# Performance work log

Hardware: AMD Instinct MI355X
Metric: run time of the kernel (lower is better)

The kernel has to match this reference:

```python
import jax, jax.numpy as jnp
import numpy as np

H_DIM = 768
N_HEADS = 12
SEQ = 4096
MLP_RATIO = 4
EPS = 1e-5


def layernorm(x, g, b):
    mu = jnp.mean(x, axis=-1, keepdims=True)
    var = jnp.var(x, axis=-1, keepdims=True)
    return (x - mu) * jax.lax.rsqrt(var + EPS) * g + b


def setup_inputs() -> dict:
    key = jax.random.key(0)
    ks = jax.random.split(key, 16)
    C, F = H_DIM, MLP_RATIO * H_DIM
    s = 1.0 / np.sqrt(C)
    inp = {
        "x": jax.random.normal(ks[0], (1, SEQ, C), dtype=jnp.float32),
        "Wq": jax.random.normal(ks[1], (C, C), dtype=jnp.float32) * s,
        "bq": jnp.zeros((C,), jnp.float32),
        "Wk": jax.random.normal(ks[2], (C, C), dtype=jnp.float32) * s,
        "bk": jnp.zeros((C,), jnp.float32),
        "Wv": jax.random.normal(ks[3], (C, C), dtype=jnp.float32) * s,
        "bv": jnp.zeros((C,), jnp.float32),
        "Wo": jax.random.normal(ks[4], (C, C), dtype=jnp.float32) * s,
        "bo": jnp.zeros((C,), jnp.float32),
        "ln1_g": jnp.ones((C,), jnp.float32),
        "ln1_b": jnp.zeros((C,), jnp.float32),
        "W1": jax.random.normal(ks[5], (C, F), dtype=jnp.float32) * s,
        "b1": jnp.zeros((F,), jnp.float32),
        "W2": jax.random.normal(ks[6], (F, C), dtype=jnp.float32) * (1.0 / np.sqrt(F)),
        "b2": jnp.zeros((C,), jnp.float32),
        "ln2_g": jnp.ones((C,), jnp.float32),
        "ln2_b": jnp.zeros((C,), jnp.float32),
    }
    return inp


def reference(x, Wq, bq, Wk, bk, Wv, bv, Wo, bo, ln1_g, ln1_b, W1, b1, W2, b2, ln2_g, ln2_b):
    B, T, C = x.shape
    N, D = N_HEADS, C // N_HEADS

    # --- masked self-attention (naive, materializes T x T scores) ---
    q = (x @ Wq + bq).reshape(B, T, N, D).transpose(0, 2, 1, 3)  # [B,N,T,D]
    k = (x @ Wk + bk).reshape(B, T, N, D).transpose(0, 2, 1, 3)
    v = (x @ Wv + bv).reshape(B, T, N, D).transpose(0, 2, 1, 3)

    logits = jnp.einsum("bntd,bnsd->bnts", q, k) / jnp.sqrt(jnp.float32(D))
    causal = jnp.tril(jnp.ones((T, T), dtype=bool))  # True where allowed
    logits = jnp.where(causal, logits, -jnp.inf)
    attn = jax.nn.softmax(logits, axis=-1)
    out = jnp.einsum("bnts,bnsd->bntd", attn, v)
    out = out.transpose(0, 2, 1, 3).reshape(B, T, C)
    attn_out = out @ Wo + bo

    # --- post-norm residual + MLP ---
    h = layernorm(x + attn_out, ln1_g, ln1_b)
    mlp = jax.nn.gelu(h @ W1 + b1, approximate=False) @ W2 + b2
    y = layernorm(h + mlp, ln2_g, ln2_b)
    return y
```

## Files before the change

### kernel.cpp

```cpp
#include <hip/hip_runtime.h>
#include <hip/hip_bf16.h>
#include <math.h>

#define T_SEQ 4096
#define C_DIM 768
#define N_HEADS 12
#define D_HEAD 64
#define F_DIM 3072
#define EPS 1e-5f
#define QSCALE 0.18033688011112042f

typedef __attribute__((ext_vector_type(8))) short short8;
typedef __attribute__((ext_vector_type(4))) float f32x4;

__device__ __forceinline__ void gload_lds16(const void* g, void* lds) {
    __builtin_amdgcn_global_load_lds(
        (const __attribute__((address_space(1))) unsigned int*)g,
        (__attribute__((address_space(3))) unsigned int*)lds, 16, 0, 0);
}

__launch_bounds__(256)
__global__ void transpose_w4(const float* __restrict__ Wq, const float* __restrict__ Wk,
                             const float* __restrict__ Wv, const float* __restrict__ Wo,
                             __hip_bfloat16* __restrict__ Wqkv_t,
                             __hip_bfloat16* __restrict__ Wo_t) {
    __shared__ float tile[64][65];
    const int z = blockIdx.z;
    const float* W = (z == 0) ? Wq : (z == 1) ? Wk : (z == 2) ? Wv : Wo;
    __hip_bfloat16* Wt = (z < 3) ? (Wqkv_t + (size_t)z * C_DIM * C_DIM) : Wo_t;
    const int k0 = blockIdx.x * 64;
    const int n0 = blockIdx.y * 64;
    const int tid = threadIdx.x;
    const int c = tid & 63;
    const int r0 = (tid >> 6) * 16;
    #pragma unroll
    for (int i = 0; i < 16; ++i)
        tile[r0 + i][c] = W[(size_t)(k0 + r0 + i) * C_DIM + n0 + c];
    __syncthreads();
    #pragma unroll
    for (int i = 0; i < 16; ++i)
        Wt[(size_t)(n0 + r0 + i) * C_DIM + k0 + c] = __float2bfloat16(tile[c][r0 + i]);
}

__launch_bounds__(256)
__global__ void transpose_w(const float* __restrict__ W, __hip_bfloat16* __restrict__ Wt,
                            int K, int N) {
    __shared__ float tile[64][65];
    const int k0 = blockIdx.x * 64;
    const int n0 = blockIdx.y * 64;
    const int tid = threadIdx.x;
    const int c = tid & 63;
    const int r0 = (tid >> 6) * 16;
    #pragma unroll
    for (int i = 0; i < 16; ++i)
        tile[r0 + i][c] = W[(size_t)(k0 + r0 + i) * N + n0 + c];
    __syncthreads();
    #pragma unroll
    for (int i = 0; i < 16; ++i)
        Wt[(size_t)(n0 + r0 + i) * K + k0 + c] = __float2bfloat16(tile[c][r0 + i]);
}

__launch_bounds__(256)
__global__ void transpose_v(const __hip_bfloat16* __restrict__ V,
                            __hip_bfloat16* __restrict__ Vt) {
    __shared__ __hip_bfloat16 tile[64][65];
    const int t0 = blockIdx.x * 64;
    const int c0 = blockIdx.y * 64;
    const int tid = threadIdx.x;
    const int c = tid & 63;
    const int r0 = (tid >> 6) * 16;
    #pragma unroll
    for (int i = 0; i < 16; ++i)
        tile[r0 + i][c] = V[(size_t)(t0 + r0 + i) * C_DIM + c0 + c];
    __syncthreads();
    #pragma unroll
    for (int i = 0; i < 16; ++i)
        Vt[(size_t)(c0 + r0 + i) * T_SEQ + t0 + c] = tile[c][r0 + i];
}

__launch_bounds__(256)
__global__ void concat_bias(const float* __restrict__ bq, const float* __restrict__ bk,
                            const float* __restrict__ bv, float* __restrict__ o) {
    const int i = blockIdx.x * 256 + threadIdx.x;
    if (i < C_DIM) {
        o[i] = bq[i];
        o[C_DIM + i] = bk[i];
        o[2 * C_DIM + i] = bv[i];
    }
}

__launch_bounds__(256)
__global__ void f32_to_bf16_vec(const float* __restrict__ in, __hip_bfloat16* __restrict__ out,
                                int n4) {
    const int i = blockIdx.x * 256 + threadIdx.x;
    if (i < n4) {
        const float4 v = *reinterpret_cast<const float4*>(&in[(size_t)i * 4]);
        ushort4 u;
        u.x = __bfloat16_as_ushort(__float2bfloat16(v.x));
        u.y = __bfloat16_as_ushort(__float2bfloat16(v.y));
        u.z = __bfloat16_as_ushort(__float2bfloat16(v.z));
        u.w = __bfloat16_as_ushort(__float2bfloat16(v.w));
        *reinterpret_cast<ushort4*>(&out[(size_t)i * 4]) = u;
    }
}

#define GBK 64

template<int MODE, int TM, int TN>
__launch_bounds__(256)
__global__ void gemm_mfma(const __hip_bfloat16* __restrict__ A,
                          const __hip_bfloat16* __restrict__ Bt,
                          const float* __restrict__ bias,
                          float* __restrict__ outf,
                          __hip_bfloat16* __restrict__ outq,
                          __hip_bfloat16* __restrict__ outk,
                          __hip_bfloat16* __restrict__ outv,
                          int M, int N, int K) {
    constexpr int WM = TM / 2, WN = TN / 2;
    constexpr int FM = WM / 16, FN = WN / 16;
    constexpr int AISS = TM / 32, BISS = TN / 32;

    __shared__ __hip_bfloat16 As[TM][GBK];
    __shared__ __hip_bfloat16 Bs[TN][GBK];

    const int tid = threadIdx.x;
    const int l   = tid & 63;
    const int w   = tid >> 6;
    const int lr  = l & 15;
    const int lg  = l >> 4;
    const int wr  = w >> 1;
    const int wc  = w & 1;
    const int bm  = blockIdx.y * TM;
    const int bn  = blockIdx.x * TN;

    const int srow  = l >> 3;
    const int skoff = (l & 7) * 8;

    f32x4 acc[FM][FN];
    #pragma unroll
    for (int m = 0; m < FM; ++m)
        #pragma unroll
        for (int n = 0; n < FN; ++n)
            acc[m][n] = {0.f, 0.f, 0.f, 0.f};

    for (int k0 = 0; k0 < K; k0 += GBK) {
        if (k0) __syncthreads();
        #pragma unroll
        for (int i = 0; i < AISS; ++i) {
            const int rb = (w * AISS + i) * 8;
            gload_lds16(&A[(size_t)(bm + rb + srow) * K + k0 + skoff], &As[rb][0]);
        }
        #pragma unroll
        for (int i = 0; i < BISS; ++i) {
            const int rb = (w * BISS + i) * 8;
            gload_lds16(&Bt[(size_t)(bn + rb + srow) * K + k0 + skoff], &Bs[rb][0]);
        }
        __syncthreads();

        #pragma unroll
        for (int kk = 0; kk < 2; ++kk) {
            short8 af[FM], bf[FN];
            #pragma unroll
            for (int m = 0; m < FM; ++m)
                af[m] = *reinterpret_cast<const short8*>(
                    &As[wr * WM + m * 16 + lr][kk * 32 + lg * 8]);
            #pragma unroll
            for (int n = 0; n < FN; ++n)
                bf[n] = *reinterpret_cast<const short8*>(
                    &Bs[wc * WN + n * 16 + lr][kk * 32 + lg * 8]);
            #pragma unroll
            for (int m = 0; m < FM; ++m)
                #pragma unroll
                for (int n = 0; n < FN; ++n)
                    acc[m][n] = __builtin_amdgcn_mfma_f32_16x16x32_bf16(af[m], bf[n], acc[m][n], 0, 0, 0);
        }
    }

    #pragma unroll
    for (int m = 0; m < FM; ++m) {
        #pragma unroll
        for (int rr = 0; rr < 4; ++rr) {
            const int row = bm + wr * WM + m * 16 + lg * 4 + rr;
            #pragma unroll
            for (int n = 0; n < FN; ++n) {
                const int col = bn + wc * WN + n * 16 + lr;
                float v = acc[m][n][rr] + bias[col];
                if constexpr (MODE == 0) {
                    outf[(size_t)row * N + col] = v;
                } else if constexpr (MODE == 1) {
                    v = 0.5f * v * (1.0f + erff(v * 0.70710678118654752f));
                    outq[(size_t)row * N + col] = __float2bfloat16(v);
                } else {
                    if (col < C_DIM)
                        outq[(size_t)row * C_DIM + col] = __float2bfloat16(v * QSCALE);
                    else if (col < 2 * C_DIM)
                        outk[(size_t)row * C_DIM + (col - C_DIM)] = __float2bfloat16(v);
                    else
                        outv[(size_t)row * C_DIM + (col - 2 * C_DIM)] = __float2bfloat16(v);
                }
            }
        }
    }
}

#define QBLK 64
#define KVB 128

__launch_bounds__(256)
__global__ void attn_mfma(const __hip_bfloat16* __restrict__ q,
                          const __hip_bfloat16* __restrict__ k,
                          const __hip_bfloat16* __restrict__ vt,
                          __hip_bfloat16* __restrict__ o) {
    __shared__ __hip_bfloat16 Ks[2][KVB][64];
    __shared__ __hip_bfloat16 Vts[2][D_HEAD][KVB];
    __shared__ __hip_bfloat16 Ps[4][16][KVB];

    const int tid  = threadIdx.x;
    const int wid  = tid >> 6;
    const int lane = tid & 63;
    const int lr   = lane & 15;
    const int lg   = lane >> 4;

    const int h  = blockIdx.x;
    const int q0 = T_SEQ - QBLK - blockIdx.y * QBLK;
    const int qw = q0 + wid * 16;

    const int ksrc = 8 * ((lane & 7) ^ (lane >> 3));
    const int kr   = lane >> 3;
    const int vr   = lane >> 4;
    const int vs   = lane & 15;

    short8 aq[2];
    #pragma unroll
    for (int kk = 0; kk < 2; ++kk)
        aq[kk] = *reinterpret_cast<const short8*>(
            &q[(size_t)(qw + lr) * C_DIM + h * D_HEAD + kk * 32 + lg * 8]);

    f32x4 o_acc[4];
    #pragma unroll
    for (int dc = 0; dc < 4; ++dc) o_acc[dc] = {0.f, 0.f, 0.f, 0.f};
    float m_run[4], l_part[4];
    #pragma unroll
    for (int r = 0; r < 4; ++r) { m_run[r] = -1e30f; l_part[r] = 0.f; }

    auto stage = [&](int buf, int s0) {
        #pragma unroll
        for (int i = 0; i < 4; ++i) {
            const int rb = wid * 32 + i * 8;
            gload_lds16(&k[(size_t)(s0 + rb + kr) * C_DIM + h * D_HEAD + ksrc],
                        &Ks[buf][rb][0]);
        }
        #pragma unroll
        for (int i = 0; i < 4; ++i) {
            const int vb = wid * 16 + i * 4;
            const int vsrc = 8 * (vs ^ (i * 4 + vr));
            gload_lds16(&vt[(size_t)(h * D_HEAD + vb + vr) * T_SEQ + s0 + vsrc],
                        &Vts[buf][vb][0]);
        }
    };

    const int n_tiles = (q0 + QBLK + KVB - 1) / KVB;

    stage(0, 0);
    __syncthreads();

    for (int t = 0; t < n_tiles; ++t) {
        const int cur = t & 1;
        if (t + 1 < n_tiles) stage(cur ^ 1, (t + 1) * KVB);

        f32x4 s_acc[8];
        __builtin_amdgcn_s_setprio(1);
        #pragma unroll
        for (int c = 0; c < 8; ++c) {
            s_acc[c] = {0.f, 0.f, 0.f, 0.f};
            #pragma unroll
            for (int kk = 0; kk < 2; ++kk) {
                const short8 bk8 = *reinterpret_cast<const short8*>(
                    &Ks[cur][c * 16 + lr][8 * ((4 * kk + lg) ^ (lr & 7))]);
                s_acc[c] = __builtin_amdgcn_mfma_f32_16x16x32_bf16(aq[kk], bk8, s_acc[c], 0, 0, 0);
            }
        }
        __builtin_amdgcn_s_setprio(0);

        if (t == n_tiles - 1) {
            const int s0 = t * KVB;
            #pragma unroll
            for (int c = 0; c < 8; ++c)
                #pragma unroll
                for (int r = 0; r < 4; ++r) {
                    const int sg = s0 + c * 16 + lr;
                    const int qg = qw + lg * 4 + r;
                    if (sg > qg) s_acc[c][r] = -1e30f;
                }
        }

        float pm[4];
        #pragma unroll
        for (int r = 0; r < 4; ++r) {
            const float m0 = fmaxf(fmaxf(s_acc[0][r], s_acc[1][r]),
                                   fmaxf(s_acc[2][r], s_acc[3][r]));
            const float m1 = fmaxf(fmaxf(s_acc[4][r], s_acc[5][r]),
                                   fmaxf(s_acc[6][r], s_acc[7][r]));
            pm[r] = fmaxf(m0, m1);
        }
        const float need = fmaxf(fmaxf(pm[0] - m_run[0], pm[1] - m_run[1]),
                                 fmaxf(pm[2] - m_run[2], pm[3] - m_run[3]));
        if (!__all(need <= 8.0f)) {
            #pragma unroll
            for (int r = 0; r < 4; ++r) {
                float nm = pm[r];
                #pragma unroll
                for (int off = 1; off < 16; off <<= 1)
                    nm = fmaxf(nm, __shfl_xor(nm, off));
                nm = fmaxf(nm, m_run[r]);
                const float corr = __builtin_amdgcn_exp2f(m_run[r] - nm);
                m_run[r] = nm;
                l_part[r] *= corr;
                #pragma unroll
                for (int dc = 0; dc < 4; ++dc) o_acc[dc][r] *= corr;
            }
        }
        #pragma unroll
        for (int r = 0; r < 4; ++r) {
            const int qrow = lg * 4 + r;
            float ls = 0.f;
            #pragma unroll
            for (int c = 0; c < 8; ++c) {
                const float pv = __builtin_amdgcn_exp2f(s_acc[c][r] - m_run[r]);
                ls += pv;
                const int slot = (2 * c + (lr >> 3)) ^ qrow;
                Ps[wid][qrow][slot * 8 + (lr & 7)] = __float2bfloat16(pv);
            }
            l_part[r] += ls;
        }

        short8 ap[4];
        #pragma unroll
        for (int kk = 0; kk < 4; ++kk)
            ap[kk] = *reinterpret_cast<const short8*>(
                &Ps[wid][lr][8 * ((4 * kk + lg) ^ lr)]);
        __builtin_amdgcn_s_setprio(1);
        #pragma unroll
        for (int dc = 0; dc < 4; ++dc)
            #pragma unroll
            for (int kk = 0; kk < 4; ++kk) {
                const short8 bv8 = *reinterpret_cast<const short8*>(
                    &Vts[cur][dc * 16 + lr][8 * ((4 * kk + lg) ^ lr)]);
                o_acc[dc] = __builtin_amdgcn_mfma_f32_16x16x32_bf16(ap[kk], bv8, o_acc[dc], 0, 0, 0);
            }
        __builtin_amdgcn_s_setprio(0);

        __syncthreads();
    }

    #pragma unroll
    for (int r = 0; r < 4; ++r) {
        #pragma unroll
        for (int off = 1; off < 16; off <<= 1)
            l_part[r] += __shfl_xor(l_part[r], off);
    }

    #pragma unroll
    for (int dc = 0; dc < 4; ++dc)
        #pragma unroll
        for (int r = 0; r < 4; ++r)
            o[(size_t)(qw + lg * 4 + r) * C_DIM + h * D_HEAD + dc * 16 + lr] =
                __float2bfloat16(o_acc[dc][r] / l_part[r]);
}

template<bool WB16>
__launch_bounds__(256)
__global__ void add_ln(const float* __restrict__ a, const float* __restrict__ b,
                       const float* __restrict__ g, const float* __restrict__ beta,
                       float* __restrict__ outf, __hip_bfloat16* __restrict__ outb) {
    const int row = blockIdx.x;
    const int tid = threadIdx.x;
    const size_t rb = (size_t)row * C_DIM;

    float x[3];
    #pragma unroll
    for (int i = 0; i < 3; ++i) {
        const int c = tid + 256 * i;
        x[i] = a[rb + c] + b[rb + c];
    }

    float s = x[0] + x[1] + x[2];
    float s2 = x[0] * x[0] + x[1] * x[1] + x[2] * x[2];

    #pragma unroll
    for (int off = 32; off; off >>= 1) {
        s  += __shfl_xor(s, off);
        s2 += __shfl_xor(s2, off);
    }

    __shared__ float red[10];
    const int wave = tid >> 6;
    const int lane = tid & 63;
    if (lane == 0) { red[wave] = s; red[4 + wave] = s2; }
    __syncthreads();
    if (tid == 0) {
        const float ts  = red[0] + red[1] + red[2] + red[3];
        const float ts2 = red[4] + red[5] + red[6] + red[7];
        const float mu = ts * (1.0f / C_DIM);
        const float var = ts2 * (1.0f / C_DIM) - mu * mu;
        red[8] = mu;
        red[9] = rsqrtf(var + EPS);
    }
    __syncthreads();
    const float mu = red[8];
    const float rstd = red[9];

    #pragma unroll
    for (int i = 0; i < 3; ++i) {
        const int c = tid + 256 * i;
        const float v = (x[i] - mu) * rstd * g[c] + beta[c];
        outf[rb + c] = v;
        if constexpr (WB16) outb[rb + c] = __float2bfloat16(v);
    }
}

extern "C" void kernel_launch(void* const* d_in, const int* in_sizes, int n_in,
                              void* d_out, int out_size, void* d_ws, size_t ws_size,
                              hipStream_t stream) {
    const float* x     = (const float*)d_in[0];
    const float* Wq    = (const float*)d_in[1];
    const float* bq    = (const float*)d_in[2];
    const float* Wk    = (const float*)d_in[3];
    const float* bk    = (const float*)d_in[4];
    const float* Wv    = (const float*)d_in[5];
    const float* bv    = (const float*)d_in[6];
    const float* Wo    = (const float*)d_in[7];
    const float* bo    = (const float*)d_in[8];
    const float* ln1_g = (const float*)d_in[9];
    const float* ln1_b = (const float*)d_in[10];
    const float* W1    = (const float*)d_in[11];
    const float* b1    = (const float*)d_in[12];
    const float* W2    = (const float*)d_in[13];
    const float* b2    = (const float*)d_in[14];
    const float* ln2_g = (const float*)d_in[15];
    const float* ln2_b = (const float*)d_in[16];

    float* out = (float*)d_out;

    char* wsb = (char*)d_ws;
    const size_t TCb16 = (size_t)T_SEQ * C_DIM * 2;
    __hip_bfloat16* xb  = (__hip_bfloat16*)(wsb);
    __hip_bfloat16* qb  = (__hip_bfloat16*)(wsb + TCb16);
    __hip_bfloat16* kb  = (__hip_bfloat16*)(wsb + 2 * TCb16);
    __hip_bfloat16* vtb = (__hip_bfloat16*)(wsb + 3 * TCb16);
    __hip_bfloat16* mid = (__hip_bfloat16*)(wsb);
    float* proj = (float*)(wsb + 4 * TCb16);
    __hip_bfloat16* vb = (__hip_bfloat16*)proj;
    float* mlpo = proj;
    __hip_bfloat16* obuf = (__hip_bfloat16*)(wsb + 4 * TCb16 + 12582912);
    __hip_bfloat16* hb   = obuf;
    float* hbuf = (float*)(wsb + 4 * TCb16 + 12582912 + TCb16);
    char* we = wsb + 4 * TCb16 + 12582912 + TCb16 + 12582912;
    __hip_bfloat16* Wqkv_t = (__hip_bfloat16*)(we);
    __hip_bfloat16* Wo_t   = (__hip_bfloat16*)(we + 3538944);
    __hip_bfloat16* W1_t   = (__hip_bfloat16*)(we + 3538944 + 1179648);
    __hip_bfloat16* W2_t   = (__hip_bfloat16*)(we + 3538944 + 1179648 + 4718592);
    float* bqkv            = (float*)(we + 3538944 + 1179648 + 2 * 4718592);

    const dim3 blk256(256);

    transpose_w4<<<dim3(12, 12, 4), blk256, 0, stream>>>(Wq, Wk, Wv, Wo, Wqkv_t, Wo_t);
    transpose_w<<<dim3(12, 48), blk256, 0, stream>>>(W1, W1_t, C_DIM, F_DIM);
    transpose_w<<<dim3(48, 12), blk256, 0, stream>>>(W2, W2_t, F_DIM, C_DIM);
    concat_bias<<<dim3(3), blk256, 0, stream>>>(bq, bk, bv, bqkv);
    f32_to_bf16_vec<<<dim3(3072), blk256, 0, stream>>>(x, xb, T_SEQ * C_DIM / 4);

    gemm_mfma<2, 128, 128><<<dim3(3 * C_DIM / 128, T_SEQ / 128), blk256, 0, stream>>>(
        xb, Wqkv_t, bqkv, nullptr, qb, kb, vb, T_SEQ, 3 * C_DIM, C_DIM);

    transpose_v<<<dim3(T_SEQ / 64, C_DIM / 64), blk256, 0, stream>>>(vb, vtb);

    attn_mfma<<<dim3(N_HEADS, T_SEQ / QBLK), blk256, 0, stream>>>(qb, kb, vtb, obuf);

    gemm_mfma<0, 64, 64><<<dim3(C_DIM / 64, T_SEQ / 64), blk256, 0, stream>>>(
        obuf, Wo_t, bo, proj, nullptr, nullptr, nullptr, T_SEQ, C_DIM, C_DIM);

    add_ln<true><<<dim3(T_SEQ), blk256, 0, stream>>>(x, proj, ln1_g, ln1_b, hbuf, hb);

    gemm_mfma<1, 128, 128><<<dim3(F_DIM / 128, T_SEQ / 128), blk256, 0, stream>>>(
        hb, W1_t, b1, nullptr, mid, nullptr, nullptr, T_SEQ, F_DIM, C_DIM);

    gemm_mfma<0, 64, 64><<<dim3(C_DIM / 64, T_SEQ / 64), blk256, 0, stream>>>(
        mid, W2_t, b2, mlpo, nullptr, nullptr, nullptr, T_SEQ, C_DIM, F_DIM);

    add_ln<false><<<dim3(T_SEQ), blk256, 0, stream>>>(hbuf, mlpo, ln2_g, ln2_b, out, nullptr);
}
```

Measured before the change: 336.3 us.

## Fuse prep kernels, add split-K to output GEMMs, and XCD-swizzle block order

The weight transposes, x conversion and bias concat are merged into one prep_all launch, which removes several small launches. The Wo and W2 GEMMs (N=768) now use split-K=2 with two fp32 partial buffers that add_ln sums, which doubles the block count. The QKV and W1 GEMMs remap block IDs across 8 chunks, which looks aimed at MI355X's XCD round-robin dispatch so that blocks sharing A/B tiles run on the same L2. The cost is extra fp32 partial-buffer traffic and a larger workspace.

```diff
diff --git a/kernel.cpp b/kernel.cpp
--- a/kernel.cpp
+++ b/kernel.cpp
@@ -20,44 +20,58 @@
 }
 
 __launch_bounds__(256)
-__global__ void transpose_w4(const float* __restrict__ Wq, const float* __restrict__ Wk,
-                             const float* __restrict__ Wv, const float* __restrict__ Wo,
-                             __hip_bfloat16* __restrict__ Wqkv_t,
-                             __hip_bfloat16* __restrict__ Wo_t) {
-    __shared__ float tile[64][65];
-    const int z = blockIdx.z;
-    const float* W = (z == 0) ? Wq : (z == 1) ? Wk : (z == 2) ? Wv : Wo;
-    __hip_bfloat16* Wt = (z < 3) ? (Wqkv_t + (size_t)z * C_DIM * C_DIM) : Wo_t;
-    const int k0 = blockIdx.x * 64;
-    const int n0 = blockIdx.y * 64;
+__global__ void prep_all(const float* __restrict__ Wq, const float* __restrict__ Wk,
+                         const float* __restrict__ Wv, const float* __restrict__ Wo,
+                         const float* __restrict__ W1, const float* __restrict__ W2,
+                         const float* __restrict__ x,
+                         const float* __restrict__ bq, const float* __restrict__ bk,
+                         const float* __restrict__ bv,
+                         __hip_bfloat16* __restrict__ Wqkv_t, __hip_bfloat16* __restrict__ Wo_t,
+                         __hip_bfloat16* __restrict__ W1_t, __hip_bfloat16* __restrict__ W2_t,
+                         __hip_bfloat16* __restrict__ xb, float* __restrict__ bqkv) {
+    const int b = blockIdx.x;
     const int tid = threadIdx.x;
-    const int c = tid & 63;
-    const int r0 = (tid >> 6) * 16;
-    #pragma unroll
-    for (int i = 0; i < 16; ++i)
-        tile[r0 + i][c] = W[(size_t)(k0 + r0 + i) * C_DIM + n0 + c];
-    __syncthreads();
-    #pragma unroll
-    for (int i = 0; i < 16; ++i)
-        Wt[(size_t)(n0 + r0 + i) * C_DIM + k0 + c] = __float2bfloat16(tile[c][r0 + i]);
-}
-
-__launch_bounds__(256)
-__global__ void transpose_w(const float* __restrict__ W, __hip_bfloat16* __restrict__ Wt,
-                            int K, int N) {
-    __shared__ float tile[64][65];
-    const int k0 = blockIdx.x * 64;
-    const int n0 = blockIdx.y * 64;
-    const int tid = threadIdx.x;
-    const int c = tid & 63;
-    const int r0 = (tid >> 6) * 16;
-    #pragma unroll
-    for (int i = 0; i < 16; ++i)
-        tile[r0 + i][c] = W[(size_t)(k0 + r0 + i) * N + n0 + c];
-    __syncthreads();
-    #pragma unroll
-    for (int i = 0; i < 16; ++i)
-        Wt[(size_t)(n0 + r0 + i) * K + k0 + c] = __float2bfloat16(tile[c][r0 + i]);
+    if (b < 1728) {
+        __shared__ float tile[64][65];
+        const float* W; __hip_bfloat16* Wt; int K, N, kx, ny;
+        if (b < 576) {
+            const int z = b / 144, t = b % 144;
+            kx = t % 12; ny = t / 12; K = C_DIM; N = C_DIM;
+            W  = (z == 0) ? Wq : (z == 1) ? Wk : (z == 2) ? Wv : Wo;
+            Wt = (z < 3) ? (Wqkv_t + (size_t)z * C_DIM * C_DIM) : Wo_t;
+        } else if (b < 1152) {
+            const int t = b - 576; kx = t % 12; ny = t / 12;
+            K = C_DIM; N = F_DIM; W = W1; Wt = W1_t;
+        } else {
+            const int t = b - 1152; kx = t % 48; ny = t / 48;
+            K = F_DIM; N = C_DIM; W = W2; Wt = W2_t;
+        }
+        const int k0 = kx * 64, n0 = ny * 64;
+        const int c = tid & 63, r0 = (tid >> 6) * 16;
+        #pragma unroll
+        for (int i = 0; i < 16; ++i)
+            tile[r0 + i][c] = W[(size_t)(k0 + r0 + i) * N + n0 + c];
+        __syncthreads();
+        #pragma unroll
+        for (int i = 0; i < 16; ++i)
+            Wt[(size_t)(n0 + r0 + i) * K + k0 + c] = __float2bfloat16(tile[c][r0 + i]);
+    } else if (b < 4800) {
+        const int i = (b - 1728) * 256 + tid;
+        const float4 v = *reinterpret_cast<const float4*>(&x[(size_t)i * 4]);
+        ushort4 u;
+        u.x = __bfloat16_as_ushort(__float2bfloat16(v.x));
+        u.y = __bfloat16_as_ushort(__float2bfloat16(v.y));
+        u.z = __bfloat16_as_ushort(__float2bfloat16(v.z));
+        u.w = __bfloat16_as_ushort(__float2bfloat16(v.w));
+        *reinterpret_cast<ushort4*>(&xb[(size_t)i * 4]) = u;
+    } else {
+        const int i = (b - 4800) * 256 + tid;
+        if (i < C_DIM) {
+            bqkv[i] = bq[i];
+            bqkv[C_DIM + i] = bk[i];
+            bqkv[2 * C_DIM + i] = bv[i];
+        }
+    }
 }
 
 __launch_bounds__(256)
@@ -78,35 +92,9 @@
         Vt[(size_t)(c0 + r0 + i) * T_SEQ + t0 + c] = tile[c][r0 + i];
 }
 
-__launch_bounds__(256)
-__global__ void concat_bias(const float* __restrict__ bq, const float* __restrict__ bk,
-                            const float* __restrict__ bv, float* __restrict__ o) {
-    const int i = blockIdx.x * 256 + threadIdx.x;
-    if (i < C_DIM) {
-        o[i] = bq[i];
-        o[C_DIM + i] = bk[i];
-        o[2 * C_DIM + i] = bv[i];
-    }
-}
-
-__launch_bounds__(256)
-__global__ void f32_to_bf16_vec(const float* __restrict__ in, __hip_bfloat16* __restrict__ out,
-                                int n4) {
-    const int i = blockIdx.x * 256 + threadIdx.x;
-    if (i < n4) {
-        const float4 v = *reinterpret_cast<const float4*>(&in[(size_t)i * 4]);
-        ushort4 u;
-        u.x = __bfloat16_as_ushort(__float2bfloat16(v.x));
-        u.y = __bfloat16_as_ushort(__float2bfloat16(v.y));
-        u.z = __bfloat16_as_ushort(__float2bfloat16(v.z));
-        u.w = __bfloat16_as_ushort(__float2bfloat16(v.w));
-        *reinterpret_cast<ushort4*>(&out[(size_t)i * 4]) = u;
-    }
-}
-
 #define GBK 64
 
-template<int MODE, int TM, int TN>
+template<int MODE, int TM, int TN, int SPLITK, bool SWZ>
 __launch_bounds__(256)
 __global__ void gemm_mfma(const __hip_bfloat16* __restrict__ A,
                           const __hip_bfloat16* __restrict__ Bt,
@@ -130,8 +118,19 @@
     const int lg  = l >> 4;
     const int wr  = w >> 1;
     const int wc  = w & 1;
-    const int bm  = blockIdx.y * TM;
-    const int bn  = blockIdx.x * TN;
+
+    int bid = blockIdx.y * gridDim.x + blockIdx.x;
+    if constexpr (SWZ) {
+        const int nwg = gridDim.x * gridDim.y;
+        const int cpx = nwg >> 3;
+        bid = (bid & 7) * cpx + (bid >> 3);
+    }
+    const int bm = (bid / gridDim.x) * TM;
+    const int bn = (bid % gridDim.x) * TN;
+
+    const int kz   = (SPLITK > 1) ? blockIdx.z : 0;
+    const int kbeg = kz * (K / SPLITK);
+    const int kend = kbeg + K / SPLITK;
 
     const int srow  = l >> 3;
     const int skoff = (l & 7) * 8;
@@ -143,8 +142,8 @@
         for (int n = 0; n < FN; ++n)
             acc[m][n] = {0.f, 0.f, 0.f, 0.f};
 
-    for (int k0 = 0; k0 < K; k0 += GBK) {
-        if (k0) __syncthreads();
+    for (int k0 = kbeg; k0 < kend; k0 += GBK) {
+        if (k0 != kbeg) __syncthreads();
         #pragma unroll
         for (int i = 0; i < AISS; ++i) {
             const int rb = (w * AISS + i) * 8;
@@ -184,9 +183,9 @@
             #pragma unroll
             for (int n = 0; n < FN; ++n) {
                 const int col = bn + wc * WN + n * 16 + lr;
-                float v = acc[m][n][rr] + bias[col];
+                float v = acc[m][n][rr] + ((SPLITK == 1 || kz == 0) ? bias[col] : 0.f);
                 if constexpr (MODE == 0) {
-                    outf[(size_t)row * N + col] = v;
+                    outf[(size_t)kz * M * N + (size_t)row * N + col] = v;
                 } else if constexpr (MODE == 1) {
                     v = 0.5f * v * (1.0f + erff(v * 0.70710678118654752f));
                     outq[(size_t)row * N + col] = __float2bfloat16(v);
@@ -370,7 +369,8 @@
 
 template<bool WB16>
 __launch_bounds__(256)
-__global__ void add_ln(const float* __restrict__ a, const float* __restrict__ b,
+__global__ void add_ln(const float* __restrict__ a, const float* __restrict__ b0,
+                       const float* __restrict__ b1,
                        const float* __restrict__ g, const float* __restrict__ beta,
                        float* __restrict__ outf, __hip_bfloat16* __restrict__ outb) {
     const int row = blockIdx.x;
@@ -381,7 +381,7 @@
     #pragma unroll
     for (int i = 0; i < 3; ++i) {
         const int c = tid + 256 * i;
-        x[i] = a[rb + c] + b[rb + c];
+        x[i] = a[rb + c] + b0[rb + c] + b1[rb + c];
     }
 
     float s = x[0] + x[1] + x[2];
@@ -444,18 +444,21 @@
 
     char* wsb = (char*)d_ws;
     const size_t TCb16 = (size_t)T_SEQ * C_DIM * 2;
+    const size_t TCf32 = (size_t)T_SEQ * C_DIM * 4;
     __hip_bfloat16* xb  = (__hip_bfloat16*)(wsb);
     __hip_bfloat16* qb  = (__hip_bfloat16*)(wsb + TCb16);
     __hip_bfloat16* kb  = (__hip_bfloat16*)(wsb + 2 * TCb16);
     __hip_bfloat16* vtb = (__hip_bfloat16*)(wsb + 3 * TCb16);
     __hip_bfloat16* mid = (__hip_bfloat16*)(wsb);
-    float* proj = (float*)(wsb + 4 * TCb16);
-    __hip_bfloat16* vb = (__hip_bfloat16*)proj;
-    float* mlpo = proj;
-    __hip_bfloat16* obuf = (__hip_bfloat16*)(wsb + 4 * TCb16 + 12582912);
+    float* proj0 = (float*)(wsb + 4 * TCb16);
+    float* proj1 = (float*)(wsb + 4 * TCb16 + TCf32);
+    __hip_bfloat16* vb = (__hip_bfloat16*)proj0;
+    float* mlpo0 = proj0;
+    float* mlpo1 = proj1;
+    __hip_bfloat16* obuf = (__hip_bfloat16*)(wsb + 4 * TCb16 + 2 * TCf32);
     __hip_bfloat16* hb   = obuf;
-    float* hbuf = (float*)(wsb + 4 * TCb16 + 12582912 + TCb16);
-    char* we = wsb + 4 * TCb16 + 12582912 + TCb16 + 12582912;
+    float* hbuf = (float*)(wsb + 4 * TCb16 + 2 * TCf32 + TCb16);
+    char* we = wsb + 4 * TCb16 + 2 * TCf32 + TCb16 + TCf32;
     __hip_bfloat16* Wqkv_t = (__hip_bfloat16*)(we);
     __hip_bfloat16* Wo_t   = (__hip_bfloat16*)(we + 3538944);
     __hip_bfloat16* W1_t   = (__hip_bfloat16*)(we + 3538944 + 1179648);
@@ -464,29 +467,26 @@
 
     const dim3 blk256(256);
 
-    transpose_w4<<<dim3(12, 12, 4), blk256, 0, stream>>>(Wq, Wk, Wv, Wo, Wqkv_t, Wo_t);
-    transpose_w<<<dim3(12, 48), blk256, 0, stream>>>(W1, W1_t, C_DIM, F_DIM);
-    transpose_w<<<dim3(48, 12), blk256, 0, stream>>>(W2, W2_t, F_DIM, C_DIM);
-    concat_bias<<<dim3(3), blk256, 0, stream>>>(bq, bk, bv, bqkv);
-    f32_to_bf16_vec<<<dim3(3072), blk256, 0, stream>>>(x, xb, T_SEQ * C_DIM / 4);
-
-    gemm_mfma<2, 128, 128><<<dim3(3 * C_DIM / 128, T_SEQ / 128), blk256, 0, stream>>>(
+    prep_all<<<dim3(4803), blk256, 0, stream>>>(Wq, Wk, Wv, Wo, W1, W2, x, bq, bk, bv,
+                                                Wqkv_t, Wo_t, W1_t, W2_t, xb, bqkv);
+
+    gemm_mfma<2, 128, 128, 1, true><<<dim3(18, 32), blk256, 0, stream>>>(
         xb, Wqkv_t, bqkv, nullptr, qb, kb, vb, T_SEQ, 3 * C_DIM, C_DIM);
 
     transpose_v<<<dim3(T_SEQ / 64, C_DIM / 64), blk256, 0, stream>>>(vb, vtb);
 
     attn_mfma<<<dim3(N_HEADS, T_SEQ / QBLK), blk256, 0, stream>>>(qb, kb, vtb, obuf);
 
-    gemm_mfma<0, 64, 64><<<dim3(C_DIM / 64, T_SEQ / 64), blk256, 0, stream>>>(
-        obuf, Wo_t, bo, proj, nullptr, nullptr, nullptr, T_SEQ, C_DIM, C_DIM);
-
-    add_ln<true><<<dim3(T_SEQ), blk256, 0, stream>>>(x, proj, ln1_g, ln1_b, hbuf, hb);
-
-    gemm_mfma<1, 128, 128><<<dim3(F_DIM / 128, T_SEQ / 128), blk256, 0, stream>>>(
+    gemm_mfma<0, 64, 64, 2, false><<<dim3(12, 64, 2), blk256, 0, stream>>>(
+        obuf, Wo_t, bo, proj0, nullptr, nullptr, nullptr, T_SEQ, C_DIM, C_DIM);
+
+    add_ln<true><<<dim3(T_SEQ), blk256, 0, stream>>>(x, proj0, proj1, ln1_g, ln1_b, hbuf, hb);
+
+    gemm_mfma<1, 128, 128, 1, true><<<dim3(24, 32), blk256, 0, stream>>>(
         hb, W1_t, b1, nullptr, mid, nullptr, nullptr, T_SEQ, F_DIM, C_DIM);
 
-    gemm_mfma<0, 64, 64><<<dim3(C_DIM / 64, T_SEQ / 64), blk256, 0, stream>>>(
-        mid, W2_t, b2, mlpo, nullptr, nullptr, nullptr, T_SEQ, C_DIM, F_DIM);
-
-    add_ln<false><<<dim3(T_SEQ), blk256, 0, stream>>>(hbuf, mlpo, ln2_g, ln2_b, out, nullptr);
-}
+    gemm_mfma<0, 64, 64, 2, false><<<dim3(12, 64, 2), blk256, 0, stream>>>(
+        mid, W2_t, b2, mlpo0, nullptr, nullptr, nullptr, T_SEQ, C_DIM, F_DIM);
+
+    add_ln<false><<<dim3(T_SEQ), blk256, 0, stream>>>(hbuf, mlpo0, mlpo1, ln2_g, ln2_b, out, nullptr);
+}
```

After: 318.6 us. -5.3%, faster.
